# Kernel optimization log

Hardware: AMD Instinct MI355X
Metric: run time of the kernel (lower is better)

The kernel has to match this reference:

```python
import jax, jax.numpy as jnp
import numpy as np

B, C, T, H, F, KS = 8, 512, 1024, 8, 2048, 3
K = C // H            # head channels = 64
ROPE_D = K // 2       # RoPE rotates half the head channels = 32
EPS = 1e-4


def setup_inputs() -> dict:
    key = jax.random.key(0)
    ks = jax.random.split(key, 12)
    s = 1.0 / np.sqrt(C)
    sf = 1.0 / np.sqrt(F)
    return {
        "x": jax.random.normal(ks[0], (B, C, T), jnp.float32),
        "x_mask": jnp.ones((B, 1, T), jnp.float32),
        "attn_mask": jnp.ones((B, 1, T, T), jnp.float32),
        "wq": jax.random.normal(ks[1], (C, C), jnp.float32) * s,
        "bq": jnp.zeros((C,), jnp.float32),
        "wk": jax.random.normal(ks[2], (C, C), jnp.float32) * s,
        "bk": jnp.zeros((C,), jnp.float32),
        "wv": jax.random.normal(ks[3], (C, C), jnp.float32) * s,
        "bv": jnp.zeros((C,), jnp.float32),
        "wo": jax.random.normal(ks[4], (C, C), jnp.float32) * s,
        "bo": jnp.zeros((C,), jnp.float32),
        "w1": jax.random.normal(ks[5], (F, C, KS), jnp.float32) * s,
        "b1": jnp.zeros((F,), jnp.float32),
        "w2": jax.random.normal(ks[6], (C, F, KS), jnp.float32) * sf,
        "b2": jnp.zeros((C,), jnp.float32),
        "g1": jnp.ones((C,), jnp.float32),
        "be1": jnp.zeros((C,), jnp.float32),
        "g2": jnp.ones((C,), jnp.float32),
        "be2": jnp.zeros((C,), jnp.float32),
    }


def _rope(x):
    # x: (B, H, T, K); rotate first ROPE_D channels, pass the rest through.
    t = x.shape[2]
    theta = 1.0 / (10000.0 ** (jnp.arange(0, ROPE_D, 2, dtype=jnp.float32) / ROPE_D))
    idx = jnp.arange(t, dtype=jnp.float32)[:, None] * theta[None, :]  # (T, d/2)
    idx2 = jnp.concatenate([idx, idx], axis=-1)                       # (T, d)
    cos, sin = jnp.cos(idx2), jnp.sin(idx2)                           # broadcast over B,H
    xr, xp = x[..., :ROPE_D], x[..., ROPE_D:]
    h = ROPE_D // 2
    neg = jnp.concatenate([-xr[..., h:], xr[..., :h]], axis=-1)
    return jnp.concatenate([xr * cos + neg * sin, xp], axis=-1)


def _ln(x, gamma, beta):
    # channel-wise LayerNorm over dim 1 of (B, C, T), eps=1e-4
    mean = jnp.mean(x, axis=1, keepdims=True)
    var = jnp.mean((x - mean) ** 2, axis=1, keepdims=True)
    xn = (x - mean) * jax.lax.rsqrt(var + EPS)
    return xn * gamma[None, :, None] + beta[None, :, None]


def _conv1d(x, w, b):
    # x: (B, Cin, T), w: (Cout, Cin, KS), 'same' padding (KS//2)
    y = jax.lax.conv_general_dilated(
        x, w, window_strides=(1,), padding=[(KS // 2, KS // 2)],
        dimension_numbers=("NCH", "OIH", "NCH"))
    return y + b[None, :, None]


def _forward(x, x_mask, attn_mask, wq, bq, wk, bk, wv, bv, wo, bo,
             w1, b1, w2, b2, g1, be1, g2, be2):
    x = x * x_mask
    # 1x1 conv projections == channel matmuls
    q = jnp.einsum("oc,bct->bot", wq, x) + bq[None, :, None]
    k = jnp.einsum("oc,bct->bot", wk, x) + bk[None, :, None]
    v = jnp.einsum("oc,bct->bot", wv, x) + bv[None, :, None]
    # (B, C, T) -> (B, H, T, K)
    def heads(a):
        return a.reshape(B, H, K, T).transpose(0, 1, 3, 2)
    q, k, v = heads(q), heads(k), heads(v)
    q = _rope(q)
    k = _rope(k)
    scores = jnp.einsum("bhtk,bhsk->bhts", q, k) / jnp.sqrt(jnp.float32(K))
    scores = jnp.where(attn_mask == 0, jnp.float32(-10000.0), scores)
    p = jax.nn.softmax(scores, axis=-1)
    o = jnp.einsum("bhts,bhsk->bhtk", p, v)              # (B,H,T,K)
    o = o.transpose(0, 1, 3, 2).reshape(B, C, T)
    y = jnp.einsum("oc,bct->bot", wo, o) + bo[None, :, None]
    x = _ln(x + y, g1, be1)
    # conv FFN
    h1 = jax.nn.relu(_conv1d(x * x_mask, w1, b1))
    y = _conv1d(h1 * x_mask, w2, b2) * x_mask
    x = _ln(x + y, g2, be2)
    return x


def reference(x, x_mask, attn_mask, wq, bq, wk, bk, wv, bv, wo, bo,
              w1, b1, w2, b2, g1, be1, g2, be2):
    return _forward(x, x_mask, attn_mask, wq, bq, wk, bk, wv, bv, wo, bo,
                    w1, b1, w2, b2, g1, be1, g2, be2)
```

## Files before the change

### kernel.cpp

```cpp
#include <hip/hip_runtime.h>

typedef unsigned short u16;
typedef __attribute__((ext_vector_type(4))) float floatx4;
typedef __attribute__((ext_vector_type(8))) __bf16 bf16x8;
typedef __attribute__((ext_vector_type(4))) unsigned short ushort4v;
typedef __attribute__((ext_vector_type(8))) unsigned short ushort8v;

#define DI __device__ __forceinline__


DI u16 f2bf(float f) {
  union { float f; unsigned u; } v; v.f = f;
  unsigned r = v.u + 0x7fffu + ((v.u >> 16) & 1u);
  return (u16)(r >> 16);
}
DI float bf2f(u16 h) {
  union { unsigned u; float f; } v; v.u = ((unsigned)h) << 16;
  return v.f;
}

#define GLDS(g, l) __builtin_amdgcn_global_load_lds( \
    (const __attribute__((address_space(1))) unsigned int*)(g), \
    (__attribute__((address_space(3))) unsigned int*)(l), 16, 0, 0)

__global__ __launch_bounds__(256, 2) void k_fattn(
    const u16* __restrict__ qb, const u16* __restrict__ kb,
    const u16* __restrict__ vb, const unsigned* __restrict__ mb,
    u16* __restrict__ oT)
{
  __shared__ __align__(16) u16 Ps[4][32 * 64];
  const int tid  = threadIdx.x;
  const int wave = tid >> 6, lane = tid & 63;
  const int lr = lane & 15, kg = lane >> 4;
  const int qt = blockIdx.x, bh = blockIdx.y;
  const int bb = bh >> 3, hh = bh & 7;
  const int wq0 = qt * 128 + wave * 32;
  const float L2E = 1.44269504f;

  const u16* Qp = qb + (size_t)bh * 65536;
  const u16* Kp = kb + (size_t)bh * 65536;
  const u16* Vp = vb + (size_t)bh * 65536;
  u16* Pw = &Ps[wave][0];

  bf16x8 qf[2][2];
#pragma unroll
  for (int i = 0; i < 2; ++i)
#pragma unroll
    for (int h = 0; h < 2; ++h)
      qf[i][h] = *(const bf16x8*)&Qp[(wq0 + i * 16 + lr) * 64 + h * 32 + kg * 8];

  float l_b[2] = {0.f, 0.f};
  floatx4 o_acc[2][4];
#pragma unroll
  for (int i = 0; i < 2; ++i)
#pragma unroll
    for (int j = 0; j < 4; ++j) o_acc[i][j] = (floatx4){0.f, 0.f, 0.f, 0.f};

  bf16x8 kf[4][2], vf[4][2];
#pragma unroll
  for (int a = 0; a < 4; ++a)
#pragma unroll
    for (int h = 0; h < 2; ++h)
      kf[a][h] = *(const bf16x8*)&Kp[(a * 16 + lr) * 64 + h * 32 + kg * 8];

  unsigned mw[2][2];
#pragma unroll
  for (int b = 0; b < 2; ++b) {
    const size_t rw = ((size_t)bb << 15) + ((size_t)(wq0 + b * 16 + lr) << 5);
    mw[b][0] = mb[rw]; mw[b][1] = mb[rw + 1];
  }

  for (int it = 0; it < 16; ++it) {
    const int s0 = it * 64;
    floatx4 sT[4][2];
    __builtin_amdgcn_s_setprio(1);
#pragma unroll
    for (int a = 0; a < 4; ++a) {
      sT[a][0] = (floatx4){0.f, 0.f, 0.f, 0.f};
      sT[a][1] = (floatx4){0.f, 0.f, 0.f, 0.f};
#pragma unroll
      for (int b = 0; b < 2; ++b)
#pragma unroll
        for (int h = 0; h < 2; ++h)
          sT[a][b] = __builtin_amdgcn_mfma_f32_16x16x32_bf16(kf[a][h], qf[b][h], sT[a][b], 0, 0, 0);
    }
    __builtin_amdgcn_s_setprio(0);
#pragma unroll
    for (int a = 0; a < 4; ++a)
#pragma unroll
      for (int h = 0; h < 2; ++h)
        vf[a][h] = *(const bf16x8*)&Vp[(a * 16 + lr) * 1024 + s0 + h * 32 + kg * 8];
    unsigned mwn[2][2];
    if (it < 15) {
      const int sn = s0 + 64;
#pragma unroll
      for (int a = 0; a < 4; ++a)
#pragma unroll
        for (int h = 0; h < 2; ++h)
          kf[a][h] = *(const bf16x8*)&Kp[(sn + a * 16 + lr) * 64 + h * 32 + kg * 8];
#pragma unroll
      for (int b = 0; b < 2; ++b) {
        const size_t rw = ((size_t)bb << 15) + ((size_t)(wq0 + b * 16 + lr) << 5) + (sn >> 5);
        mwn[b][0] = mb[rw]; mwn[b][1] = mb[rw + 1];
      }
    }
#pragma unroll
    for (int b = 0; b < 2; ++b) {
      float sum = 0.f;
#pragma unroll
      for (int a = 0; a < 4; ++a)
#pragma unroll
        for (int r = 0; r < 4; ++r) {
          const int sl = a * 16 + kg * 4 + r;
          float sv = sT[a][b][r];
          const unsigned wsel = (sl & 32) ? mw[b][1] : mw[b][0];
          if (!((wsel >> (sl & 31)) & 1u)) sv = -10000.f;
          const float p = exp2f(sv * L2E);
          sT[a][b][r] = p;
          sum += p;
        }
      l_b[b] += sum;
#pragma unroll
      for (int a = 0; a < 4; ++a) {
        ushort4v pk;
#pragma unroll
        for (int r = 0; r < 4; ++r) {
          __bf16 hv = (__bf16)sT[a][b][r];
          pk[r] = *(u16*)&hv;
        }
        const int sl0 = a * 16 + kg * 4;
        *(ushort4v*)&Pw[(b * 16 + lr) * 64 + (sl0 ^ ((lr & 7) << 3))] = pk;
      }
    }
    if (it < 15) {
#pragma unroll
      for (int b = 0; b < 2; ++b) { mw[b][0] = mwn[b][0]; mw[b][1] = mwn[b][1]; }
    }
    asm volatile("s_waitcnt lgkmcnt(0)" ::: "memory");
    __builtin_amdgcn_sched_barrier(0);
    bf16x8 pa[2][2];
#pragma unroll
    for (int i = 0; i < 2; ++i)
#pragma unroll
      for (int h = 0; h < 2; ++h)
        pa[i][h] = *(const bf16x8*)&Pw[(i * 16 + lr) * 64 + (((h * 4 + kg) ^ (lr & 7)) << 3)];
    __builtin_amdgcn_s_setprio(1);
#pragma unroll
    for (int jd = 0; jd < 4; ++jd)
#pragma unroll
      for (int i = 0; i < 2; ++i)
#pragma unroll
        for (int h = 0; h < 2; ++h)
          o_acc[i][jd] = __builtin_amdgcn_mfma_f32_16x16x32_bf16(pa[i][h], vf[jd][h], o_acc[i][jd], 0, 0, 0);
    __builtin_amdgcn_s_setprio(0);
  }
#pragma unroll
  for (int i = 0; i < 2; ++i) {
    l_b[i] += __shfl_xor(l_b[i], 16);
    l_b[i] += __shfl_xor(l_b[i], 32);
  }
  float linv[2][4];
#pragma unroll
  for (int i = 0; i < 2; ++i)
#pragma unroll
    for (int r = 0; r < 4; ++r) linv[i][r] = 1.f / __shfl(l_b[i], kg * 4 + r);
#pragma unroll
  for (int i = 0; i < 2; ++i)
#pragma unroll
    for (int jd = 0; jd < 4; ++jd)
#pragma unroll
      for (int r = 0; r < 4; ++r) {
        const int t = wq0 + i * 16 + kg * 4 + r;
        const int c = hh * 64 + jd * 16 + lr;
        oT[((size_t)bb * 1024 + t) * 512 + c] = f2bf(o_acc[i][jd][r] * linv[i][r]);
      }
}

template<int MODE, int BN, int TAPK>
__global__ __launch_bounds__(256) void k_cgemm(
    const u16* __restrict__ A, int lda,
    const u16* __restrict__ Bsrc, int ldb,
    int K,
    u16* __restrict__ o0, u16* __restrict__ o1, u16* __restrict__ o2,
    const float* __restrict__ bias,
    const float* __restrict__ ctab, const float* __restrict__ stab,
    const float* __restrict__ msk)
{
  constexpr int BM = 128;
  constexpr int FN = BN / 32;
  __shared__ __align__(16) u16 As[2 * BM * 32];
  __shared__ __align__(16) u16 Bs[2 * BN * 32];

  const int tid  = threadIdx.x;
  const int wave = tid >> 6, lane = tid & 63;
  const int wm = wave >> 1, wn = wave & 1;
  const int lr = lane & 15, kg = lane >> 4;

  const int nwg = gridDim.x * gridDim.y;
  const int h0  = blockIdx.y * gridDim.x + blockIdx.x;
  const int cpx = nwg >> 3;
  const int tl  = (h0 & 7) * cpx + (h0 >> 3);
  const int bx  = tl % gridDim.x;
  const int by  = tl / gridDim.x;

  const int m0 = bx * BM, n0 = by * BN;
  const int koff = blockIdx.z * K;

  const u16* aP[2][BM / 64];
  const u16* bP[2][BN / 64];
#pragma unroll
  for (int h = 0; h < 2; ++h) {
#pragma unroll
    for (int ch = 0; ch < BM / 64; ++ch) {
      const int idx = ch * 256 + tid;
      const int row = idx >> 2;
      const int kk = (((idx & 3) ^ ((row >> 1) & 3)) << 3);
      aP[h][ch] = A + (size_t)(m0 + row) * lda + koff + h * 32 + kk;
    }
#pragma unroll
    for (int ch = 0; ch < BN / 64; ++ch) {
      const int idx = ch * 256 + tid;
      const int row = idx >> 2;
      const int kk = (((idx & 3) ^ ((row >> 1) & 3)) << 3);
      const int bt = n0 + row;
      size_t rowbase;
      if constexpr (TAPK == 0) {
        rowbase = (size_t)bt * ldb;
      } else {
        const int b = bt >> 10, t = bt & 1023;
        rowbase = ((size_t)(b * 1026 + t)) * TAPK;
      }
      bP[h][ch] = Bsrc + rowbase + koff + h * 32 + kk;
    }
  }

  floatx4 acc[4][FN];
#pragma unroll
  for (int i = 0; i < 4; ++i)
#pragma unroll
    for (int j = 0; j < FN; ++j) acc[i][j] = (floatx4){0.f, 0.f, 0.f, 0.f};

  const int csw = (kg ^ ((lr >> 1) & 3)) * 8;

  for (int k0 = 0; k0 < K; k0 += 64) {
#pragma unroll
    for (int h = 0; h < 2; ++h) {
#pragma unroll
      for (int ch = 0; ch < BM / 64; ++ch)
        GLDS(aP[h][ch] + k0, &As[h * BM * 32 + (ch * 256 + tid) * 8]);
#pragma unroll
      for (int ch = 0; ch < BN / 64; ++ch)
        GLDS(bP[h][ch] + k0, &Bs[h * BN * 32 + (ch * 256 + tid) * 8]);
    }
    __syncthreads();
    bf16x8 af[2][4], bfr[2][FN];
#pragma unroll
    for (int h = 0; h < 2; ++h) {
#pragma unroll
      for (int i = 0; i < 4; ++i)
        af[h][i] = *(const bf16x8*)&As[(h * BM + wm * 64 + i * 16 + lr) * 32 + csw];
#pragma unroll
      for (int j = 0; j < FN; ++j)
        bfr[h][j] = *(const bf16x8*)&Bs[(h * BN + wn * (BN / 2) + j * 16 + lr) * 32 + csw];
    }
#pragma unroll
    for (int h = 0; h < 2; ++h)
#pragma unroll
      for (int i = 0; i < 4; ++i)
#pragma unroll
        for (int j = 0; j < FN; ++j)
          acc[i][j] = __builtin_amdgcn_mfma_f32_16x16x32_bf16(af[h][i], bfr[h][j], acc[i][j], 0, 0, 0);
    __syncthreads();
  }

  const int wrow0 = m0 + wm * 64;
  const int col0  = n0 + wn * (BN / 2);

  if constexpr (MODE == 0) {
    float v[4][FN][4];
#pragma unroll
    for (int i = 0; i < 4; ++i)
#pragma unroll
      for (int j = 0; j < FN; ++j)
#pragma unroll
        for (int r = 0; r < 4; ++r)
          v[i][j][r] = acc[i][j][r] + bias[wrow0 + i * 16 + kg * 4 + r];
    const int sec = wrow0 >> 9;
    const int hh  = (wrow0 & 511) >> 6;
    if (sec < 2) {
      if (sec == 0) {
#pragma unroll
        for (int i = 0; i < 4; ++i)
#pragma unroll
          for (int j = 0; j < FN; ++j)
#pragma unroll
            for (int r = 0; r < 4; ++r) v[i][j][r] *= 0.125f;
      }
#pragma unroll
      for (int j = 0; j < FN; ++j) {
        const int t = (col0 + j * 16 + lr) & 1023;
#pragma unroll
        for (int r = 0; r < 4; ++r) {
          const int a = kg * 4 + r;
          const float cv = ctab[t * 16 + a], sv = stab[t * 16 + a];
          const float a0 = v[0][j][r], a1 = v[1][j][r];
          v[0][j][r] = a0 * cv - a1 * sv;
          v[1][j][r] = a1 * cv + a0 * sv;
        }
      }
      u16* dst = (sec == 0) ? o0 : o1;
#pragma unroll
      for (int i = 0; i < 4; ++i)
#pragma unroll
        for (int j = 0; j < FN; ++j) {
          const int bt = col0 + j * 16 + lr;
          const int b = bt >> 10, t = bt & 1023;
          ushort4v pk;
#pragma unroll
          for (int r = 0; r < 4; ++r) pk[r] = f2bf(v[i][j][r]);
          *(ushort4v*)&dst[(((size_t)b * 8 + hh) * 1024 + t) * 64 + i * 16 + kg * 4] = pk;
        }
    } else {
#pragma unroll
      for (int i = 0; i < 4; ++i)
#pragma unroll
        for (int j = 0; j < FN; ++j) {
          const int bt = col0 + j * 16 + lr;
          const int b = bt >> 10, t = bt & 1023;
#pragma unroll
          for (int r = 0; r < 4; ++r) {
            const int dk = i * 16 + kg * 4 + r;
            o2[(((size_t)b * 8 + hh) * 64 + dk) * 1024 + t] = f2bf(v[i][j][r]);
          }
        }
    }
  } else if constexpr (MODE == 3) {
#pragma unroll
    for (int i = 0; i < 4; ++i)
#pragma unroll
      for (int j = 0; j < FN; ++j) {
        const int bt = col0 + j * 16 + lr;
        const int c0 = wrow0 + i * 16 + kg * 4;
        ushort4v pk;
#pragma unroll
        for (int r = 0; r < 4; ++r) pk[r] = f2bf(acc[i][j][r] + bias[c0 + r]);
        *(ushort4v*)&o0[(size_t)bt * 512 + c0] = pk;
      }
  } else if constexpr (MODE == 4) {
#pragma unroll
    for (int i = 0; i < 4; ++i) {
      const int r0 = wrow0 + i * 16 + kg * 4;
#pragma unroll
      for (int j = 0; j < FN; ++j) {
        const int bt = col0 + j * 16 + lr;
        const int b = bt >> 10, t = bt & 1023;
        const float mv = msk[(size_t)b * 1024 + t];
        ushort4v pk;
#pragma unroll
        for (int r = 0; r < 4; ++r)
          pk[r] = f2bf(fmaxf(acc[i][j][r] + bias[r0 + r], 0.f) * mv);
        *(ushort4v*)&o0[((size_t)(b * 1026 + t + 1)) * 2048 + r0] = pk;
      }
    }
  } else {
    u16* dst = o0 + (size_t)blockIdx.z * 8 * 1024 * 512;
    const bool z0 = (blockIdx.z == 0);
#pragma unroll
    for (int i = 0; i < 4; ++i)
#pragma unroll
      for (int j = 0; j < FN; ++j) {
        const int bt = col0 + j * 16 + lr;
        const int b = bt >> 10, t = bt & 1023;
        const int c0 = wrow0 + i * 16 + kg * 4;
        const float mv = msk[(size_t)b * 1024 + t];
        ushort4v pk;
#pragma unroll
        for (int r = 0; r < 4; ++r) {
          const float bv = z0 ? bias[c0 + r] : 0.f;
          pk[r] = f2bf((acc[i][j][r] + bv) * mv);
        }
        *(ushort4v*)&dst[(size_t)bt * 512 + c0] = pk;
      }
  }
}

__global__ __launch_bounds__(256) void k_prep(
    const float* __restrict__ wq, const float* __restrict__ wk,
    const float* __restrict__ wv, const float* __restrict__ wo,
    const float* __restrict__ w1, const float* __restrict__ w2,
    const float* __restrict__ bq, const float* __restrict__ bk,
    const float* __restrict__ bv, const float* __restrict__ am,
    const float* __restrict__ x, const float* __restrict__ xm,
    u16* __restrict__ wqkv, u16* __restrict__ wob,
    u16* __restrict__ w1p, u16* __restrict__ w2p,
    float* __restrict__ bqkv, float* __restrict__ ctab, float* __restrict__ stab,
    unsigned* __restrict__ mbits, u16* __restrict__ x2p, u16* __restrict__ h1p,
    u16* __restrict__ xbT)
{
  __shared__ u16 tile[64][65];
  const int bid = blockIdx.x;
  if (bid < 4096) {
    const int seg = bid >> 10;
    const int i = (bid & 1023) * 256 + threadIdx.x;
    const float* src = (seg == 0) ? wq : (seg == 1) ? wk : (seg == 2) ? wv : wo;
    u16* dst = (seg < 3) ? (wqkv + (size_t)seg * 512 * 512) : wob;
    dst[i] = f2bf(src[i]);
  } else if (bid < 8192) {
    const int i = (bid - 4096) * 256 + threadIdx.x;
    const int f = i >> 9, c = i & 511;
    const float* s = &w1[(size_t)f * 1536 + c * 3];
#pragma unroll
    for (int kk = 0; kk < 3; ++kk)
      w1p[(size_t)f * 1536 + kk * 512 + c] = f2bf(s[kk]);
  } else if (bid < 12288) {
    const int i = (bid - 8192) * 256 + threadIdx.x;
    const int c = i >> 11, f = i & 2047;
    const float* s = &w2[(size_t)c * 6144 + f * 3];
#pragma unroll
    for (int kk = 0; kk < 3; ++kk)
      w2p[(size_t)c * 6144 + kk * 2048 + f] = f2bf(s[kk]);
  } else if (bid < 13312) {
    const int i = (bid - 12288) * 256 + threadIdx.x;
    const float* src = am + (size_t)i * 32;
    unsigned w = 0;
#pragma unroll
    for (int q = 0; q < 32; ++q) w |= (src[q] != 0.f) ? (1u << q) : 0u;
    mbits[i] = w;
  } else if (bid < 13376) {
    const int i = (bid - 13312) * 256 + threadIdx.x;
    const int t = i >> 4, a = i & 15;
    const float theta = powf(10000.f, -(float)a / 16.f);
    const float ang = (float)t * theta;
    ctab[i] = cosf(ang);
    stab[i] = sinf(ang);
  } else if (bid == 13376) {
    for (int i = threadIdx.x; i < 1536; i += 256)
      bqkv[i] = (i < 512) ? bq[i] : (i < 1024) ? bk[i - 512] : bv[i - 1024];
  } else if (bid < 13409) {
    int zb = bid - 13377;
    if (zb < 16) {
      const int b = zb >> 1;
      const size_t row = (zb & 1) ? 1025 : 0;
      u16* r = x2p + ((size_t)b * 1026 + row) * 512;
      for (int i = threadIdx.x; i < 512; i += 256) r[i] = 0;
    } else {
      zb -= 16;
      const int b = zb >> 1;
      const size_t row = (zb & 1) ? 1025 : 0;
      u16* r = h1p + ((size_t)b * 1026 + row) * 2048;
      for (int i = threadIdx.x; i < 2048; i += 256) r[i] = 0;
    }
  } else {
    const int zb = bid - 13409;
    const int b = zb & 7, tt0 = (zb >> 3) & 15, rr0 = zb >> 7;
    const int r0 = rr0 * 64, t0 = tt0 * 64;
    const int tx = threadIdx.x & 63, ty = threadIdx.x >> 6;
    const float mv = xm[(size_t)b * 1024 + t0 + tx];
    const float* ib = x + (size_t)b * 512 * 1024;
#pragma unroll
    for (int rr = ty; rr < 64; rr += 4)
      tile[rr][tx] = f2bf(ib[(size_t)(r0 + rr) * 1024 + t0 + tx] * mv);
    __syncthreads();
    u16* ob = xbT + (size_t)b * 1024 * 512;
#pragma unroll
    for (int t2 = ty; t2 < 64; t2 += 4)
      ob[(size_t)(t0 + t2) * 512 + r0 + tx] = tile[tx][t2];
  }
}

__global__ __launch_bounds__(256) void k_ln1(
    const u16* __restrict__ xbT, const u16* __restrict__ y1T,
    const float* __restrict__ xm, const float* __restrict__ g,
    const float* __restrict__ be, u16* __restrict__ x2T, u16* __restrict__ x2p)
{
  const int lane = threadIdx.x & 63, wv = threadIdx.x >> 6;
  const int row = blockIdx.x * 4 + wv;
  const int b = row >> 10, t = row & 1023;
  const size_t base = (size_t)row * 512 + lane * 8;
  ushort8v ux = *(const ushort8v*)&xbT[base];
  ushort8v uy = *(const ushort8v*)&y1T[base];
  float v[8];
  float sum = 0.f, ss = 0.f;
#pragma unroll
  for (int q = 0; q < 8; ++q) {
    v[q] = bf2f(ux[q]) + bf2f(uy[q]);
    sum += v[q]; ss += v[q] * v[q];
  }
#pragma unroll
  for (int o = 32; o; o >>= 1) { sum += __shfl_xor(sum, o); ss += __shfl_xor(ss, o); }
  const float mean = sum * (1.f / 512.f);
  const float var  = ss * (1.f / 512.f) - mean * mean;
  const float rs   = rsqrtf(var + 1e-4f);
  const float m    = xm[(size_t)b * 1024 + t];
  ushort8v on, om;
#pragma unroll
  for (int q = 0; q < 8; ++q) {
    const int c = lane * 8 + q;
    const float nv = (v[q] - mean) * rs * g[c] + be[c];
    on[q] = f2bf(nv);
    om[q] = f2bf(nv * m);
  }
  *(ushort8v*)&x2T[base] = on;
  *(ushort8v*)&x2p[((size_t)(b * 1026 + t + 1)) * 512 + lane * 8] = om;
}

__global__ __launch_bounds__(256) void k_ln2_stats(
    const u16* __restrict__ x2T, const u16* __restrict__ c2p,
    float2* __restrict__ mr)
{
  constexpr size_t S = (size_t)8 * 1024 * 512;
  const int lane = threadIdx.x & 63, wv = threadIdx.x >> 6;
  const int row = blockIdx.x * 4 + wv;
  const size_t base = (size_t)row * 512 + lane * 8;
  ushort8v u0 = *(const ushort8v*)&x2T[base];
  ushort8v u1 = *(const ushort8v*)&c2p[base];
  ushort8v u2 = *(const ushort8v*)&c2p[S + base];
  float sum = 0.f, ss = 0.f;
#pragma unroll
  for (int q = 0; q < 8; ++q) {
    const float v = bf2f(u0[q]) + bf2f(u1[q]) + bf2f(u2[q]);
    sum += v; ss += v * v;
  }
#pragma unroll
  for (int o = 32; o; o >>= 1) { sum += __shfl_xor(sum, o); ss += __shfl_xor(ss, o); }
  if (lane == 0) {
    const float mean = sum * (1.f / 512.f);
    const float var  = ss * (1.f / 512.f) - mean * mean;
    mr[row] = (float2){mean, rsqrtf(var + 1e-4f)};
  }
}

__global__ __launch_bounds__(256) void k_ln2_write(
    const u16* __restrict__ x2T, const u16* __restrict__ c2p,
    const float2* __restrict__ mr,
    const float* __restrict__ g, const float* __restrict__ be,
    float* __restrict__ out)
{
  constexpr size_t S = (size_t)8 * 1024 * 512;
  __shared__ float tile[64][65];
  const int cc0 = blockIdx.x * 64, t0 = blockIdx.y * 64, b = blockIdx.z;
  const int tid = threadIdx.x;
  const int c4 = (tid & 15) * 4;
  const int tr = tid >> 4;
  float g4[4], b4[4];
#pragma unroll
  for (int q = 0; q < 4; ++q) { g4[q] = g[cc0 + c4 + q]; b4[q] = be[cc0 + c4 + q]; }
#pragma unroll
  for (int it = 0; it < 4; ++it) {
    const int tt = tr + it * 16;
    const int row = b * 1024 + t0 + tt;
    const size_t base = (size_t)row * 512 + cc0 + c4;
    ushort4v u0 = *(const ushort4v*)&x2T[base];
    ushort4v u1 = *(const ushort4v*)&c2p[base];
    ushort4v u2 = *(const ushort4v*)&c2p[S + base];
    const float2 s = mr[row];
#pragma unroll
    for (int q = 0; q < 4; ++q) {
      const float v = bf2f(u0[q]) + bf2f(u1[q]) + bf2f(u2[q]);
      tile[tt][c4 + q] = (v - s.x) * s.y * g4[q] + b4[q];
    }
  }
  __syncthreads();
  const int tx = tid & 63, cg = tid >> 6;
#pragma unroll
  for (int c = cg; c < 64; c += 4)
    out[((size_t)b * 512 + cc0 + c) * 1024 + t0 + tx] = tile[tx][c];
}

extern "C" void kernel_launch(void* const* d_in, const int* in_sizes, int n_in,
                              void* d_out, int out_size, void* d_ws, size_t ws_size,
                              hipStream_t stream) {
  (void)in_sizes; (void)n_in; (void)out_size; (void)ws_size;
  const float* x   = (const float*)d_in[0];
  const float* xm  = (const float*)d_in[1];
  const float* am  = (const float*)d_in[2];
  const float* wq  = (const float*)d_in[3];
  const float* bq  = (const float*)d_in[4];
  const float* wk  = (const float*)d_in[5];
  const float* bk  = (const float*)d_in[6];
  const float* wv  = (const float*)d_in[7];
  const float* bv  = (const float*)d_in[8];
  const float* wo  = (const float*)d_in[9];
  const float* bo  = (const float*)d_in[10];
  const float* w1  = (const float*)d_in[11];
  const float* b1  = (const float*)d_in[12];
  const float* w2  = (const float*)d_in[13];
  const float* b2  = (const float*)d_in[14];
  const float* g1  = (const float*)d_in[15];
  const float* be1 = (const float*)d_in[16];
  const float* g2  = (const float*)d_in[17];
  const float* be2 = (const float*)d_in[18];
  float* out = (float*)d_out;

  char* ws = (char*)d_ws;
  size_t off = 0;
  auto alloc = [&](size_t bytes) { char* p = ws + off; off += (bytes + 255) & ~(size_t)255; return p; };

  u16*   wqkv = (u16*)  alloc((size_t)1536 * 512 * 2);
  u16*   wob  = (u16*)  alloc((size_t)512 * 512 * 2);
  u16*   w1p  = (u16*)  alloc((size_t)2048 * 1536 * 2);
  u16*   w2p  = (u16*)  alloc((size_t)512 * 6144 * 2);
  float* bqkv = (float*)alloc(1536 * 4);
  float* ctab = (float*)alloc(1024 * 16 * 4);
  float* stab = (float*)alloc(1024 * 16 * 4);
  unsigned* mbits = (unsigned*)alloc((size_t)8 * 1024 * 32 * 4);
  float2* mr  = (float2*)alloc((size_t)8192 * 8);
  u16*   x2T  = (u16*)  alloc((size_t)8 * 1024 * 512 * 2);
  u16*   x2p  = (u16*)  alloc((size_t)8 * 1026 * 512 * 2);
  u16*   h1p  = (u16*)  alloc((size_t)8 * 1026 * 2048 * 2);
  u16*   y1T  = (u16*)  alloc((size_t)8 * 1024 * 512 * 2);
  u16*   xbT  = (u16*)  alloc((size_t)8 * 1024 * 512 * 2);
  u16*   oT   = (u16*)  alloc((size_t)8 * 1024 * 512 * 2);
  u16*   qkv3 = (u16*)  alloc((size_t)3 * 8 * 8 * 1024 * 64 * 2);
  u16*   c2p  = (u16*)  alloc((size_t)2 * 8 * 1024 * 512 * 2);

  u16* qb = qkv3;
  u16* kb = qkv3 + (size_t)8 * 8 * 1024 * 64;
  u16* vb = kb   + (size_t)8 * 8 * 1024 * 64;

  dim3 blk(256);

  k_prep<<<dim3(14433), blk, 0, stream>>>(
      wq, wk, wv, wo, w1, w2, bq, bk, bv, am, x, xm,
      wqkv, wob, w1p, w2p, bqkv, ctab, stab, mbits, x2p, h1p, xbT);

  k_cgemm<0, 128, 0><<<dim3(12, 64), blk, 0, stream>>>(
      wqkv, 512, xbT, 512, 512, qb, kb, vb, bqkv, ctab, stab, nullptr);

  k_fattn<<<dim3(8, 64), blk, 0, stream>>>(qb, kb, vb, mbits, oT);

  k_cgemm<3, 64, 0><<<dim3(4, 128), blk, 0, stream>>>(
      wob, 512, oT, 512, 512, y1T, nullptr, nullptr, bo, nullptr, nullptr, nullptr);

  k_ln1<<<dim3(2048), blk, 0, stream>>>(xbT, y1T, xm, g1, be1, x2T, x2p);

  k_cgemm<4, 128, 512><<<dim3(16, 64), blk, 0, stream>>>(
      w1p, 1536, x2p, 0, 1536, h1p, nullptr, nullptr, b1, nullptr, nullptr, xm);
  k_cgemm<5, 64, 2048><<<dim3(4, 128, 2), blk, 0, stream>>>(
      w2p, 6144, h1p, 0, 3072, c2p, nullptr, nullptr, b2, nullptr, nullptr, xm);

  k_ln2_stats<<<dim3(2048), blk, 0, stream>>>(x2T, c2p, mr);
  k_ln2_write<<<dim3(8, 16, 8), blk, 0, stream>>>(x2T, c2p, mr, g2, be2, out);
}
```

Measured before the change: 290.8 us.

## Add triple-buffered pipelined GEMM kernel for conv FFN layers

```diff
diff --git a/kernel.cpp b/kernel.cpp
--- a/kernel.cpp
+++ b/kernel.cpp
@@ -334,7 +334,7 @@
           }
         }
     }
-  } else if constexpr (MODE == 3) {
+  } else {
 #pragma unroll
     for (int i = 0; i < 4; ++i)
 #pragma unroll
@@ -346,7 +346,118 @@
         for (int r = 0; r < 4; ++r) pk[r] = f2bf(acc[i][j][r] + bias[c0 + r]);
         *(ushort4v*)&o0[(size_t)bt * 512 + c0] = pk;
       }
-  } else if constexpr (MODE == 4) {
+  }
+}
+
+template<int MODE, int BN, int TAPK>
+__global__ __launch_bounds__(256) void k_pgemm(
+    const u16* __restrict__ A, int lda,
+    const u16* __restrict__ Bsrc,
+    int K,
+    u16* __restrict__ o0,
+    const float* __restrict__ bias,
+    const float* __restrict__ msk)
+{
+  constexpr int BM = 128;
+  constexpr int FN = BN / 32;
+  constexpr int ACH = 2;
+  constexpr int BCH = BN * 32 / (8 * 256);
+  constexpr int LT  = ACH + BCH;
+  __shared__ __align__(16) u16 As[3][BM * 32];
+  __shared__ __align__(16) u16 Bs[3][BN * 32];
+
+  const int tid  = threadIdx.x;
+  const int wave = tid >> 6, lane = tid & 63;
+  const int wm = wave >> 1, wn = wave & 1;
+  const int lr = lane & 15, kg = lane >> 4;
+
+  const int nwg = gridDim.x * gridDim.y;
+  const int h0  = blockIdx.y * gridDim.x + blockIdx.x;
+  const int cpx = nwg >> 3;
+  const int tl  = (h0 & 7) * cpx + (h0 >> 3);
+  const int bx  = tl % gridDim.x;
+  const int by  = tl / gridDim.x;
+
+  const int m0 = bx * BM, n0 = by * BN;
+  const int koff = blockIdx.z * K;
+
+  const u16* aP[ACH];
+  const u16* bP[BCH];
+#pragma unroll
+  for (int ch = 0; ch < ACH; ++ch) {
+    const int idx = ch * 256 + tid;
+    const int row = idx >> 2;
+    const int kk = (((idx & 3) ^ ((row >> 1) & 3)) << 3);
+    aP[ch] = A + (size_t)(m0 + row) * lda + koff + kk;
+  }
+#pragma unroll
+  for (int ch = 0; ch < BCH; ++ch) {
+    const int idx = ch * 256 + tid;
+    const int row = idx >> 2;
+    const int kk = (((idx & 3) ^ ((row >> 1) & 3)) << 3);
+    const int bt = n0 + row;
+    const int b = bt >> 10, t = bt & 1023;
+    bP[ch] = Bsrc + ((size_t)(b * 1026 + t)) * TAPK + koff + kk;
+  }
+
+  auto stage = [&](int slot, int kg0) {
+#pragma unroll
+    for (int ch = 0; ch < ACH; ++ch)
+      GLDS(aP[ch] + kg0, &As[slot][(ch * 256 + tid) * 8]);
+#pragma unroll
+    for (int ch = 0; ch < BCH; ++ch)
+      GLDS(bP[ch] + kg0, &Bs[slot][(ch * 256 + tid) * 8]);
+  };
+
+  floatx4 acc[4][FN];
+#pragma unroll
+  for (int i = 0; i < 4; ++i)
+#pragma unroll
+    for (int j = 0; j < FN; ++j) acc[i][j] = (floatx4){0.f, 0.f, 0.f, 0.f};
+
+  const int csw = (kg ^ ((lr >> 1) & 3)) * 8;
+
+  const int P = K / 32;
+  stage(0, 0);
+  stage(1, 32);
+  int bsel = 0;
+  for (int p = 0; p < P; ++p) {
+    if (p + 1 < P) {
+      if constexpr (LT == 4) asm volatile("s_waitcnt vmcnt(4)" ::: "memory");
+      else                   asm volatile("s_waitcnt vmcnt(3)" ::: "memory");
+    } else {
+      asm volatile("s_waitcnt vmcnt(0)" ::: "memory");
+    }
+    __builtin_amdgcn_sched_barrier(0);
+    __builtin_amdgcn_s_barrier();
+    __builtin_amdgcn_sched_barrier(0);
+    const u16* Ab = &As[bsel][0];
+    const u16* Bb = &Bs[bsel][0];
+    bf16x8 af[4], bfr[FN];
+#pragma unroll
+    for (int i = 0; i < 4; ++i)
+      af[i] = *(const bf16x8*)&Ab[(wm * 64 + i * 16 + lr) * 32 + csw];
+#pragma unroll
+    for (int j = 0; j < FN; ++j)
+      bfr[j] = *(const bf16x8*)&Bb[(wn * (BN / 2) + j * 16 + lr) * 32 + csw];
+    if (p + 2 < P) {
+      const int slot2 = (bsel + 2 >= 3) ? bsel - 1 : bsel + 2;
+      stage(slot2, (p + 2) * 32);
+    }
+    __builtin_amdgcn_s_setprio(1);
+#pragma unroll
+    for (int i = 0; i < 4; ++i)
+#pragma unroll
+      for (int j = 0; j < FN; ++j)
+        acc[i][j] = __builtin_amdgcn_mfma_f32_16x16x32_bf16(af[i], bfr[j], acc[i][j], 0, 0, 0);
+    __builtin_amdgcn_s_setprio(0);
+    bsel = (bsel == 2) ? 0 : bsel + 1;
+  }
+
+  const int wrow0 = m0 + wm * 64;
+  const int col0  = n0 + wn * (BN / 2);
+
+  if constexpr (MODE == 4) {
 #pragma unroll
     for (int i = 0; i < 4; ++i) {
       const int r0 = wrow0 + i * 16 + kg * 4;
@@ -634,10 +745,10 @@
 
   k_ln1<<<dim3(2048), blk, 0, stream>>>(xbT, y1T, xm, g1, be1, x2T, x2p);
 
-  k_cgemm<4, 128, 512><<<dim3(16, 64), blk, 0, stream>>>(
-      w1p, 1536, x2p, 0, 1536, h1p, nullptr, nullptr, b1, nullptr, nullptr, xm);
-  k_cgemm<5, 64, 2048><<<dim3(4, 128, 2), blk, 0, stream>>>(
-      w2p, 6144, h1p, 0, 3072, c2p, nullptr, nullptr, b2, nullptr, nullptr, xm);
+  k_pgemm<4, 128, 512><<<dim3(16, 64), blk, 0, stream>>>(
+      w1p, 1536, x2p, 1536, h1p, b1, xm);
+  k_pgemm<5, 64, 2048><<<dim3(4, 128, 2), blk, 0, stream>>>(
+      w2p, 6144, h1p, 3072, c2p, b2, xm);
 
   k_ln2_stats<<<dim3(2048), blk, 0, stream>>>(x2T, c2p, mr);
   k_ln2_write<<<dim3(8, 16, 8), blk, 0, stream>>>(x2T, c2p, mr, g2, be2, out);
```

Result: slower. 301.0 us (+3.5%).
